# Kernel tuning notes

Measured on AMD Instinct MI355X. Metric: run time of the kernel, lower is better.

## Reference

```python
import jax, jax.numpy as jnp
import numpy as np

B, N, F_IN, F_OUT = 8, 2048, 128, 128


def setup_inputs() -> dict:
    key = jax.random.key(0)
    k1, k2, k3, k4 = jax.random.split(key, 4)
    h = jax.random.normal(k1, (B, N, F_IN), dtype=jnp.float32)
    adj = (jax.random.uniform(k2, (B, N, N)) > 0.5).astype(jnp.float32)
    adj = jnp.maximum(adj, jnp.eye(N, dtype=jnp.float32)[None])
    # torch nn.Linear weights: W is [out_features, in_features], a is [1, 2*out_features]
    W = jax.random.normal(k3, (F_OUT, F_IN), dtype=jnp.float32) * 0.05
    a = jax.random.normal(k4, (1, 2 * F_OUT), dtype=jnp.float32) * 0.05
    return {"h": h, "adj": adj, "W": W, "a": a}


def reference(h, adj, W, a):
    # Wh = W(h): [B, N, F_OUT]
    Wh = jnp.einsum("bnf,of->bno", h, W)
    # attn_fc(concat(Wh_i, Wh_j)) == (Wh_i @ a1) + (Wh_j @ a2): exact split of the
    # linear layer, avoiding the O(B*N*N*2F) concat intermediate.
    a1 = a[0, :F_OUT]
    a2 = a[0, F_OUT:]
    e_i = Wh @ a1  # [B, N]  score contribution of destination node i
    e_j = Wh @ a2  # [B, N]  score contribution of source node j
    e = e_i[:, :, None] + e_j[:, None, :]  # [B, N, N]
    e = e + (1.0 - adj) * (-1e9)
    alpha = jax.nn.softmax(e, axis=-1)  # [B, N, N]
    # weighted aggregation: h_out[b,i] = sum_j alpha[b,i,j] * Wh[b,j]
    h_out = jnp.einsum("bij,bjo->bio", alpha, Wh)
    return h_out
```

## Files before the change

kernel.cpp:

```cpp
#include <hip/hip_runtime.h>
#include <stdint.h>

#define AS1 __attribute__((address_space(1)))
#define AS3 __attribute__((address_space(3)))

typedef __bf16 bf16x8 __attribute__((ext_vector_type(8)));
typedef float f32x4 __attribute__((ext_vector_type(4)));

constexpr int NB = 8;
constexpr int N  = 2048;
constexpr int F  = 128;

__device__ __forceinline__ unsigned short bf16r(float f) {
    unsigned u = __float_as_uint(f);
    return (unsigned short)((u + 0x7FFFu + ((u >> 16) & 1u)) >> 16);
}
__device__ __forceinline__ float bf2f(unsigned short s) {
    return __uint_as_float(((unsigned)s) << 16);
}


__global__ __launch_bounds__(256) void k1_wh(const float* __restrict__ h,
                                             const float* __restrict__ W,
                                             const float* __restrict__ a,
                                             unsigned short* __restrict__ Wb2,
                                             unsigned short* __restrict__ p16) {
    __shared__ float epart[2][64];

    const int tid  = threadIdx.x;
    const int lane = tid & 63, wid = tid >> 6;
    const int quad = lane >> 4, l15 = lane & 15;
    const int wm = wid >> 1, wn = wid & 1;
    const int m0 = blockIdx.x * 64;
    const int batch = m0 >> 11;
    const int nbase = m0 & 2047;

    f32x4 acc[2][4] = {};

#pragma unroll
    for (int kk = 0; kk < 4; ++kk) {
        const int k = kk * 32 + quad * 8;
        bf16x8 afr[2], bfr[4];
#pragma unroll
        for (int rt = 0; rt < 2; ++rt) {
            const float* src = h + (size_t)(m0 + wm * 32 + rt * 16 + l15) * F + k;
            float4 x0 = *(const float4*)src;
            float4 x1 = *(const float4*)(src + 4);
            afr[rt][0] = (__bf16)x0.x; afr[rt][1] = (__bf16)x0.y;
            afr[rt][2] = (__bf16)x0.z; afr[rt][3] = (__bf16)x0.w;
            afr[rt][4] = (__bf16)x1.x; afr[rt][5] = (__bf16)x1.y;
            afr[rt][6] = (__bf16)x1.z; afr[rt][7] = (__bf16)x1.w;
        }
#pragma unroll
        for (int ct = 0; ct < 4; ++ct) {
            const int o = wn * 64 + ct * 16 + l15;
            const float* src = W + (size_t)o * F + k;
            float4 x0 = *(const float4*)src;
            float4 x1 = *(const float4*)(src + 4);
            bfr[ct][0] = (__bf16)x0.x; bfr[ct][1] = (__bf16)x0.y;
            bfr[ct][2] = (__bf16)x0.z; bfr[ct][3] = (__bf16)x0.w;
            bfr[ct][4] = (__bf16)x1.x; bfr[ct][5] = (__bf16)x1.y;
            bfr[ct][6] = (__bf16)x1.z; bfr[ct][7] = (__bf16)x1.w;
        }
#pragma unroll
        for (int rt = 0; rt < 2; ++rt)
#pragma unroll
            for (int ct = 0; ct < 4; ++ct)
                acc[rt][ct] = __builtin_amdgcn_mfma_f32_16x16x32_bf16(
                    afr[rt], bfr[ct], acc[rt][ct], 0, 0, 0);
    }

    float a2v[4];
#pragma unroll
    for (int ct = 0; ct < 4; ++ct) a2v[ct] = a[F + wn * 64 + ct * 16 + l15];

    float ep[2][4];
#pragma unroll
    for (int rt = 0; rt < 2; ++rt)
#pragma unroll
        for (int g = 0; g < 4; ++g) {
            float s = 0.f;
#pragma unroll
            for (int ct = 0; ct < 4; ++ct) s += acc[rt][ct][g] * a2v[ct];
            ep[rt][g] = s;
        }
#pragma unroll
    for (int m = 1; m < 16; m <<= 1)
#pragma unroll
        for (int rt = 0; rt < 2; ++rt)
#pragma unroll
            for (int g = 0; g < 4; ++g)
                ep[rt][g] += __shfl_xor(ep[rt][g], m);

    if (l15 == 0)
#pragma unroll
        for (int rt = 0; rt < 2; ++rt)
#pragma unroll
            for (int g = 0; g < 4; ++g)
                epart[wn][wm * 32 + rt * 16 + quad * 4 + g] = ep[rt][g];
    __syncthreads();

#pragma unroll
    for (int rt = 0; rt < 2; ++rt)
#pragma unroll
        for (int ct = 0; ct < 4; ++ct) {
            const int o  = wn * 64 + ct * 16 + l15;
            const int r0 = wm * 32 + rt * 16 + quad * 4;
            const int n0 = nbase + r0;
            ushort4 v;
#pragma unroll
            for (int g = 0; g < 4; ++g) {
                const float e  = epart[0][r0 + g] + epart[1][r0 + g];
                const float pf = bf2f(bf16r(expf(e)));
                (&v.x)[g] = bf16r(pf * acc[rt][ct][g]);
            }
            size_t off = (size_t)batch * N * F + (size_t)(n0 >> 3) * 1024 + o * 8 + (n0 & 7);
            *(ushort4*)&Wb2[off] = v;
        }

    if (tid < 64) {
        const float e = epart[0][tid] + epart[1][tid];
        p16[batch * N + nbase + tid] = bf16r(expf(e));
    }
}

__global__ __launch_bounds__(256) void k3_attn(const float* __restrict__ adj,
                                               const unsigned short* __restrict__ Wb2,
                                               const unsigned short* __restrict__ p16,
                                               float* __restrict__ out) {
    __shared__ __align__(16) float          At[2][16 * 64];
    __shared__ __align__(16) unsigned short Bt[2][8 * 1024];

    const int tid  = threadIdx.x;
    const int lane = tid & 63, wid = tid >> 6;
    const int quad = lane >> 4, l15 = lane & 15;
    const int b  = blockIdx.x & 7;
    const int i0 = (blockIdx.x >> 3) * 16;

    const int ri = wid * 4 + (lane >> 4);
    const int lslot = lane & 15;
    const float* aSrc = adj + (size_t)b * N * N + (size_t)(i0 + ri) * N
                      + ((lslot ^ ri) << 2);
    const char* bSrc = (const char*)Wb2 + (size_t)b * N * F * 2
                     + (size_t)wid * 4096 + lane * 16;
    const unsigned short* pb = p16 + b * N;

    auto stage = [&](int buf, int c) {
        __builtin_amdgcn_global_load_lds((const AS1 void*)(aSrc + c * 64),
            (AS3 void*)((char*)&At[buf][0] + wid * 1024), 16, 0, 0);
#pragma unroll
        for (int s = 0; s < 4; ++s)
            __builtin_amdgcn_global_load_lds(
                (const AS1 void*)(bSrc + (size_t)c * 16384 + s * 1024),
                (AS3 void*)((char*)&Bt[buf][0] + wid * 4096 + s * 1024), 16, 0, 0);
    };

    f32x4 acc[2] = {};
    f32x4 dacc = {};

    stage(0, 0);

    for (int c = 0; c < 32; ++c) {
        const int cur = c & 1;
        __syncthreads();
        if (c + 1 < 32) stage(cur ^ 1, c + 1);

#pragma unroll
        for (int ks = 0; ks < 2; ++ks) {
            const char* rowb = (const char*)&At[cur][0] + l15 * 256;
            const int g0 = ks * 8 + quad * 2;
            f32x4 x0 = *(const f32x4*)(rowb + ((g0 ^ l15) << 4));
            f32x4 x1 = *(const f32x4*)(rowb + (((g0 + 1) ^ l15) << 4));
            const char* bb = (const char*)&Bt[cur][0]
                           + (ks * 4 + quad) * 2048 + wid * 512 + l15 * 16;
            bf16x8 b0 = *(const bf16x8*)bb;
            bf16x8 b1 = *(const bf16x8*)(bb + 256);
            bf16x8 pv = *(const bf16x8*)(pb + c * 64 + ks * 32 + quad * 8);

            bf16x8 af;
            af[0] = (__bf16)x0[0]; af[1] = (__bf16)x0[1];
            af[2] = (__bf16)x0[2]; af[3] = (__bf16)x0[3];
            af[4] = (__bf16)x1[0]; af[5] = (__bf16)x1[1];
            af[6] = (__bf16)x1[2]; af[7] = (__bf16)x1[3];

            acc[0] = __builtin_amdgcn_mfma_f32_16x16x32_bf16(af, b0, acc[0], 0, 0, 0);
            acc[1] = __builtin_amdgcn_mfma_f32_16x16x32_bf16(af, b1, acc[1], 0, 0, 0);
            dacc   = __builtin_amdgcn_mfma_f32_16x16x32_bf16(af, pv, dacc, 0, 0, 0);
        }
    }

    float inv[4];
#pragma unroll
    for (int g = 0; g < 4; ++g) inv[g] = 1.0f / dacc[g];

    float* ob = out + (size_t)b * N * F;
#pragma unroll
    for (int ct = 0; ct < 2; ++ct) {
        const int o = wid * 32 + ct * 16 + l15;
#pragma unroll
        for (int g = 0; g < 4; ++g) {
            const int i = i0 + quad * 4 + g;
            ob[(size_t)i * F + o] = acc[ct][g] * inv[g];
        }
    }
}

extern "C" void kernel_launch(void* const* d_in, const int* in_sizes, int n_in,
                              void* d_out, int out_size, void* d_ws, size_t ws_size,
                              hipStream_t stream) {
    const float* h   = (const float*)d_in[0];
    const float* adj = (const float*)d_in[1];
    const float* W   = (const float*)d_in[2];
    const float* a   = (const float*)d_in[3];
    float* out = (float*)d_out;

    unsigned short* Wb2 = (unsigned short*)d_ws;
    unsigned short* p16 = (unsigned short*)((char*)d_ws + (4u << 20));

    k1_wh<<<NB * N / 64, 256, 0, stream>>>(h, W, a, Wb2, p16);
    k3_attn<<<NB * (N / 16), 256, 0, stream>>>(adj, Wb2, p16, out);
}
```

Measured before the change: 220.3 us.

## Triple-buffer attention tiles with manual vmcnt waits and stage p16 in LDS

The attention kernel goes from double to triple buffering of the adjacency and Wh tiles. The loop is unrolled by three and uses explicit s_waitcnt vmcnt/s_barrier so two chunks of global->LDS loads stay in flight instead of one. The per-batch exp(e_j) vector is loaded once into shared memory instead of being read from global memory every step. This costs more LDS per block, which may lower occupancy, and depends on the hand-counted vmcnt values being correct.

```diff
diff --git a/kernel.cpp b/kernel.cpp
--- a/kernel.cpp
+++ b/kernel.cpp
@@ -128,8 +128,9 @@
                                                const unsigned short* __restrict__ Wb2,
                                                const unsigned short* __restrict__ p16,
                                                float* __restrict__ out) {
-    __shared__ __align__(16) float          At[2][16 * 64];
-    __shared__ __align__(16) unsigned short Bt[2][8 * 1024];
+    __shared__ __align__(16) float          At[3][16 * 64];
+    __shared__ __align__(16) unsigned short Bt[3][8 * 1024];
+    __shared__ __align__(16) unsigned short Pt[2048];
 
     const int tid  = threadIdx.x;
     const int lane = tid & 63, wid = tid >> 6;
@@ -143,7 +144,8 @@
                       + ((lslot ^ ri) << 2);
     const char* bSrc = (const char*)Wb2 + (size_t)b * N * F * 2
                      + (size_t)wid * 4096 + lane * 16;
-    const unsigned short* pb = p16 + b * N;
+    const char* pSrc = (const char*)p16 + (size_t)b * N * 2
+                     + (size_t)wid * 1024 + lane * 16;
 
     auto stage = [&](int buf, int c) {
         __builtin_amdgcn_global_load_lds((const AS1 void*)(aSrc + c * 64),
@@ -158,36 +160,46 @@
     f32x4 acc[2] = {};
     f32x4 dacc = {};
 
+    __builtin_amdgcn_global_load_lds((const AS1 void*)pSrc,
+        (AS3 void*)((char*)&Pt[0] + wid * 1024), 16, 0, 0);
     stage(0, 0);
-
-    for (int c = 0; c < 32; ++c) {
-        const int cur = c & 1;
-        __syncthreads();
-        if (c + 1 < 32) stage(cur ^ 1, c + 1);
-
-#pragma unroll
-        for (int ks = 0; ks < 2; ++ks) {
-            const char* rowb = (const char*)&At[cur][0] + l15 * 256;
-            const int g0 = ks * 8 + quad * 2;
-            f32x4 x0 = *(const f32x4*)(rowb + ((g0 ^ l15) << 4));
-            f32x4 x1 = *(const f32x4*)(rowb + (((g0 + 1) ^ l15) << 4));
-            const char* bb = (const char*)&Bt[cur][0]
-                           + (ks * 4 + quad) * 2048 + wid * 512 + l15 * 16;
-            bf16x8 b0 = *(const bf16x8*)bb;
-            bf16x8 b1 = *(const bf16x8*)(bb + 256);
-            bf16x8 pv = *(const bf16x8*)(pb + c * 64 + ks * 32 + quad * 8);
-
-            bf16x8 af;
-            af[0] = (__bf16)x0[0]; af[1] = (__bf16)x0[1];
-            af[2] = (__bf16)x0[2]; af[3] = (__bf16)x0[3];
-            af[4] = (__bf16)x1[0]; af[5] = (__bf16)x1[1];
-            af[6] = (__bf16)x1[2]; af[7] = (__bf16)x1[3];
-
-            acc[0] = __builtin_amdgcn_mfma_f32_16x16x32_bf16(af, b0, acc[0], 0, 0, 0);
-            acc[1] = __builtin_amdgcn_mfma_f32_16x16x32_bf16(af, b1, acc[1], 0, 0, 0);
-            dacc   = __builtin_amdgcn_mfma_f32_16x16x32_bf16(af, pv, dacc, 0, 0, 0);
-        }
-    }
+    stage(1, 1);
+
+#define BODY(C, BUF, DOSTAGE, VMSTR) do {                                     \
+    asm volatile("s_waitcnt " VMSTR ::: "memory");                            \
+    asm volatile("s_barrier" ::: "memory");                                   \
+    if (DOSTAGE) stage(((BUF) + 2) % 3, (C) + 2);                             \
+    _Pragma("unroll")                                                         \
+    for (int ks = 0; ks < 2; ++ks) {                                          \
+        const char* rowb = (const char*)&At[BUF][0] + l15 * 256;              \
+        const int g0 = ks * 8 + quad * 2;                                     \
+        f32x4 x0 = *(const f32x4*)(rowb + ((g0 ^ l15) << 4));                 \
+        f32x4 x1 = *(const f32x4*)(rowb + (((g0 + 1) ^ l15) << 4));           \
+        const char* bb = (const char*)&Bt[BUF][0]                             \
+                       + (ks * 4 + quad) * 2048 + wid * 512 + l15 * 16;       \
+        bf16x8 b0 = *(const bf16x8*)bb;                                       \
+        bf16x8 b1 = *(const bf16x8*)(bb + 256);                               \
+        bf16x8 pv = *(const bf16x8*)((const char*)&Pt[0]                      \
+                       + (C) * 128 + ks * 64 + quad * 16);                    \
+        bf16x8 af;                                                            \
+        af[0] = (__bf16)x0[0]; af[1] = (__bf16)x0[1];                         \
+        af[2] = (__bf16)x0[2]; af[3] = (__bf16)x0[3];                         \
+        af[4] = (__bf16)x1[0]; af[5] = (__bf16)x1[1];                         \
+        af[6] = (__bf16)x1[2]; af[7] = (__bf16)x1[3];                         \
+        acc[0] = __builtin_amdgcn_mfma_f32_16x16x32_bf16(af, b0, acc[0], 0, 0, 0); \
+        acc[1] = __builtin_amdgcn_mfma_f32_16x16x32_bf16(af, b1, acc[1], 0, 0, 0); \
+        dacc   = __builtin_amdgcn_mfma_f32_16x16x32_bf16(af, pv, dacc, 0, 0, 0);   \
+    }                                                                         \
+} while (0)
+
+    for (int c0 = 0; c0 < 30; c0 += 3) {
+        BODY(c0 + 0, 0, 1, "vmcnt(5)");
+        BODY(c0 + 1, 1, 1, "vmcnt(5)");
+        BODY(c0 + 2, 2, 1, "vmcnt(5)");
+    }
+    BODY(30, 0, 0, "vmcnt(5)");
+    BODY(31, 1, 0, "vmcnt(0)");
+#undef BODY
 
     float inv[4];
 #pragma unroll
```

Result: slower. 242.9 us (+10.3%).

## Double row tile in attention kernel and stage p16 row into LDS

Applied to the files above, without the earlier changes.

The attention kernel now handles 32 destination rows per block instead of 16, with waves arranged 2x2 over rows and output columns. Each wave computes four output column tiles, so every staged Wb2 tile is reused across twice as many rows, halving Wb2 global traffic. The per-batch exp-score vector is loaded into LDS once at kernel start rather than read from global each step. The cost is more LDS and registers per block and half as many blocks (512), which may reduce occupancy on a kernel dominated by streaming the adjacency matrix.

```diff
diff --git a/kernel.cpp b/kernel.cpp
--- a/kernel.cpp
+++ b/kernel.cpp
@@ -128,26 +128,35 @@
                                                const unsigned short* __restrict__ Wb2,
                                                const unsigned short* __restrict__ p16,
                                                float* __restrict__ out) {
-    __shared__ __align__(16) float          At[2][16 * 64];
+    __shared__ __align__(16) float          At[2][32 * 64];
     __shared__ __align__(16) unsigned short Bt[2][8 * 1024];
+    __shared__ __align__(16) unsigned short Pt[2048];
 
     const int tid  = threadIdx.x;
     const int lane = tid & 63, wid = tid >> 6;
     const int quad = lane >> 4, l15 = lane & 15;
+    const int wm = wid >> 1, wn = wid & 1;
     const int b  = blockIdx.x & 7;
-    const int i0 = (blockIdx.x >> 3) * 16;
-
-    const int ri = wid * 4 + (lane >> 4);
+    const int i0 = (blockIdx.x >> 3) * 32;
+
     const int lslot = lane & 15;
-    const float* aSrc = adj + (size_t)b * N * N + (size_t)(i0 + ri) * N
-                      + ((lslot ^ ri) << 2);
+    const float* aSrcs[2];
+#pragma unroll
+    for (int s = 0; s < 2; ++s) {
+        const int ri = (wid * 2 + s) * 4 + (lane >> 4);
+        aSrcs[s] = adj + (size_t)b * N * N + (size_t)(i0 + ri) * N
+                 + ((lslot ^ (ri & 15)) << 2);
+    }
     const char* bSrc = (const char*)Wb2 + (size_t)b * N * F * 2
                      + (size_t)wid * 4096 + lane * 16;
-    const unsigned short* pb = p16 + b * N;
+    const char* pSrc = (const char*)p16 + (size_t)b * N * 2
+                     + (size_t)wid * 1024 + lane * 16;
 
     auto stage = [&](int buf, int c) {
-        __builtin_amdgcn_global_load_lds((const AS1 void*)(aSrc + c * 64),
-            (AS3 void*)((char*)&At[buf][0] + wid * 1024), 16, 0, 0);
+#pragma unroll
+        for (int s = 0; s < 2; ++s)
+            __builtin_amdgcn_global_load_lds((const AS1 void*)(aSrcs[s] + c * 64),
+                (AS3 void*)((char*)&At[buf][0] + (wid * 2 + s) * 1024), 16, 0, 0);
 #pragma unroll
         for (int s = 0; s < 4; ++s)
             __builtin_amdgcn_global_load_lds(
@@ -155,9 +164,11 @@
                 (AS3 void*)((char*)&Bt[buf][0] + wid * 4096 + s * 1024), 16, 0, 0);
     };
 
-    f32x4 acc[2] = {};
+    f32x4 acc[4] = {};
     f32x4 dacc = {};
 
+    __builtin_amdgcn_global_load_lds((const AS1 void*)pSrc,
+        (AS3 void*)((char*)&Pt[0] + wid * 1024), 16, 0, 0);
     stage(0, 0);
 
     for (int c = 0; c < 32; ++c) {
@@ -167,15 +178,18 @@
 
 #pragma unroll
         for (int ks = 0; ks < 2; ++ks) {
-            const char* rowb = (const char*)&At[cur][0] + l15 * 256;
+            const char* rowb = (const char*)&At[cur][0] + (wm * 16 + l15) * 256;
             const int g0 = ks * 8 + quad * 2;
             f32x4 x0 = *(const f32x4*)(rowb + ((g0 ^ l15) << 4));
             f32x4 x1 = *(const f32x4*)(rowb + (((g0 + 1) ^ l15) << 4));
             const char* bb = (const char*)&Bt[cur][0]
-                           + (ks * 4 + quad) * 2048 + wid * 512 + l15 * 16;
+                           + (ks * 4 + quad) * 2048 + wn * 1024 + l15 * 16;
             bf16x8 b0 = *(const bf16x8*)bb;
             bf16x8 b1 = *(const bf16x8*)(bb + 256);
-            bf16x8 pv = *(const bf16x8*)(pb + c * 64 + ks * 32 + quad * 8);
+            bf16x8 b2 = *(const bf16x8*)(bb + 512);
+            bf16x8 b3 = *(const bf16x8*)(bb + 768);
+            bf16x8 pv = *(const bf16x8*)((const char*)&Pt[0]
+                           + c * 128 + ks * 64 + quad * 16);
 
             bf16x8 af;
             af[0] = (__bf16)x0[0]; af[1] = (__bf16)x0[1];
@@ -185,6 +199,8 @@
 
             acc[0] = __builtin_amdgcn_mfma_f32_16x16x32_bf16(af, b0, acc[0], 0, 0, 0);
             acc[1] = __builtin_amdgcn_mfma_f32_16x16x32_bf16(af, b1, acc[1], 0, 0, 0);
+            acc[2] = __builtin_amdgcn_mfma_f32_16x16x32_bf16(af, b2, acc[2], 0, 0, 0);
+            acc[3] = __builtin_amdgcn_mfma_f32_16x16x32_bf16(af, b3, acc[3], 0, 0, 0);
             dacc   = __builtin_amdgcn_mfma_f32_16x16x32_bf16(af, pv, dacc, 0, 0, 0);
         }
     }
@@ -195,11 +211,11 @@
 
     float* ob = out + (size_t)b * N * F;
 #pragma unroll
-    for (int ct = 0; ct < 2; ++ct) {
-        const int o = wid * 32 + ct * 16 + l15;
+    for (int ct = 0; ct < 4; ++ct) {
+        const int o = wn * 64 + ct * 16 + l15;
 #pragma unroll
         for (int g = 0; g < 4; ++g) {
-            const int i = i0 + quad * 4 + g;
+            const int i = i0 + wm * 16 + quad * 4 + g;
             ob[(size_t)i * F + o] = acc[ct][g] * inv[g];
         }
     }
@@ -218,5 +234,5 @@
     unsigned short* p16 = (unsigned short*)((char*)d_ws + (4u << 20));
 
     k1_wh<<<NB * N / 64, 256, 0, stream>>>(h, W, a, Wb2, p16);
-    k3_attn<<<NB * (N / 16), 256, 0, stream>>>(adj, Wb2, p16, out);
-}
+    k3_attn<<<NB * (N / 32), 256, 0, stream>>>(adj, Wb2, p16, out);
+}
```

Result: no change. 218.9 us (-0.6%).
